# Kernel optimization log

Measured on AMD Instinct MI355X. Metric: run time of the kernel, lower is better.

Reference implementation:

```python
import jax, jax.numpy as jnp
import numpy as np

B, T, S, H = 8, 256, 256, 512


def setup_inputs() -> dict:
    key = jax.random.key(0)
    k1, k2, k3, k4, k5, k6, k7 = jax.random.split(key, 7)
    query = jax.random.normal(k1, (B, T, H), dtype=jnp.float32)
    encoder_outputs = jax.random.normal(k2, (B, S, H), dtype=jnp.float32)
    src_lengths = jax.random.randint(k3, (B,), 1, S + 1)
    src_lengths = src_lengths.at[0].set(S)  # ensure max(lengths) == S (torch code masks to lengths.max())
    scale = 1.0 / np.sqrt(H)
    W_s = jax.random.normal(k4, (H, H), dtype=jnp.float32) * scale      # nn.Linear(H,H) weight
    W_h = jax.random.normal(k5, (H, H), dtype=jnp.float32) * scale
    v = jax.random.normal(k6, (H,), dtype=jnp.float32) * scale          # nn.Linear(H,1) weight
    W_out = jax.random.normal(k7, (H, 2 * H), dtype=jnp.float32) * scale  # nn.Linear(2H,H) weight
    return {"query": query, "encoder_outputs": encoder_outputs, "src_lengths": src_lengths,
            "W_s": W_s, "W_h": W_h, "v": v, "W_out": W_out}


def reference(query, encoder_outputs, src_lengths, W_s, W_h, v, W_out):
    # torch Linear: y = x @ W.T
    Ws_q = jnp.einsum('bth,oh->bto', query, W_s)            # (B,T,H)
    Wh_e = jnp.einsum('bsh,oh->bso', encoder_outputs, W_h)  # (B,S,H)
    # score(i,j) = v^T tanh(Ws_q_j + Wh_e_i), broadcast over (B,T,S,H)
    energies = jnp.einsum('btsh,h->bts',
                          jnp.tanh(Ws_q[:, :, None, :] + Wh_e[:, None, :, :]), v)
    mask = jnp.arange(encoder_outputs.shape[1]) < src_lengths[:, None]  # (B,S)
    energies = jnp.where(mask[:, None, :], energies, -jnp.inf)
    attn_weights = jax.nn.softmax(energies, axis=-1)        # (B,T,S)
    context = jnp.einsum('bts,bsh->bth', attn_weights, encoder_outputs)
    combined = jnp.concatenate([context, query], axis=-1)   # (B,T,2H)
    attn_out = jnp.tanh(jnp.einsum('btk,ok->bto', combined, W_out))
    return attn_out
```

## Files before the change

### kernel.cpp

```cpp
#include <hip/hip_runtime.h>
#include <hip/hip_bf16.h>


typedef __attribute__((ext_vector_type(8))) short bf16x8;
typedef __attribute__((ext_vector_type(4))) float floatx4;

#define C2LOG2E 2.8853900817779268f
#define LOG2E   1.4426950408889634f
#define NEGBIG  -1e30f

__device__ __forceinline__ float fexp2(float x) { return __builtin_amdgcn_exp2f(x); }
__device__ __forceinline__ float frcp(float x)  { return __builtin_amdgcn_rcpf(x); }
__device__ __forceinline__ float ftanh(float x) {
    return 1.0f - 2.0f * frcp(1.0f + fexp2(C2LOG2E * x));
}

__device__ __forceinline__ unsigned int f2bf_bits(float f) {
    unsigned int u = __float_as_uint(f);
    return (u + 0x7fffu + ((u >> 16) & 1u)) >> 16;
}

__global__ __launch_bounds__(256) void cast_all_bf16(
    const float* __restrict__ q,  const float* __restrict__ e,
    const float* __restrict__ Ws, const float* __restrict__ Wh,
    const float* __restrict__ Wo,
    unsigned short* __restrict__ qb,  unsigned short* __restrict__ eb,
    unsigned short* __restrict__ Wsb, unsigned short* __restrict__ Whb,
    unsigned short* __restrict__ Wob)
{
    int blk = blockIdx.x;
    const float* src; unsigned short* dst; int base;
    if      (blk < 1024) { src = q;  dst = qb;  base = blk; }
    else if (blk < 2048) { src = e;  dst = eb;  base = blk - 1024; }
    else if (blk < 2304) { src = Ws; dst = Wsb; base = blk - 2048; }
    else if (blk < 2560) { src = Wh; dst = Whb; base = blk - 2304; }
    else                 { src = Wo; dst = Wob; base = blk - 2560; }
    size_t i = (size_t)base * 1024 + threadIdx.x * 4;
    float4 f = *(const float4*)(src + i);
    ushort4 o;
    o.x = (unsigned short)f2bf_bits(f.x);
    o.y = (unsigned short)f2bf_bits(f.y);
    o.z = (unsigned short)f2bf_bits(f.z);
    o.w = (unsigned short)f2bf_bits(f.w);
    *(ushort4*)(dst + i) = o;
}

__global__ __launch_bounds__(256) void gemm32x64_tanh_dual(
    const unsigned short* __restrict__ Xa, const unsigned short* __restrict__ Wa,
    float* __restrict__ Ca,
    const unsigned short* __restrict__ Xb, const unsigned short* __restrict__ Wb_,
    float* __restrict__ Cb)
{
    __shared__ unsigned short sA[32 * 72];
    __shared__ unsigned short sB[64 * 72];
    const int K = 512;
    int blk = blockIdx.x;
    const unsigned short* X; const unsigned short* W; float* C;
    int mt, nt, N;
    if (blk < 512) { X = Xa; W = Wa; C = Ca; N = 512;  mt = blk >> 3; nt = blk & 7; }
    else { blk -= 512; X = Xb; W = Wb_; C = Cb; N = 2048; mt = blk >> 5; nt = blk & 31; }
    int row0 = mt * 32, col0 = nt * 64;
    int tid = threadIdx.x, lane = tid & 63, w = tid >> 6;
    int srA = tid >> 3, scA = (tid & 7) * 8;
    int srB = tid >> 2, scB = (tid & 3) * 16;
    int mw = (w & 1) * 16, nw = (w >> 1) * 32;
    int r = lane & 15, kq = (lane >> 4) * 8;

    floatx4 acc0 = {0,0,0,0}, acc1 = {0,0,0,0};
    const unsigned short* ga = X + (size_t)(row0 + srA) * K + scA;
    const unsigned short* gb = W + (size_t)(col0 + srB) * K + scB;

    for (int kb = 0; kb < 8; ++kb) {
        uint4 a0 = *(const uint4*)(ga);
        uint4 b0 = *(const uint4*)(gb);
        uint4 b1 = *(const uint4*)(gb + 8);
        ga += 64; gb += 64;
        __syncthreads();
        *(uint4*)&sA[srA * 72 + scA]     = a0;
        *(uint4*)&sB[srB * 72 + scB]     = b0;
        *(uint4*)&sB[srB * 72 + scB + 8] = b1;
        __syncthreads();
#pragma unroll
        for (int ks = 0; ks < 64; ks += 32) {
            bf16x8 af  = *(const bf16x8*)&sA[(mw + r) * 72 + ks + kq];
            bf16x8 bf0 = *(const bf16x8*)&sB[(nw + r) * 72 + ks + kq];
            bf16x8 bf1 = *(const bf16x8*)&sB[(nw + 16 + r) * 72 + ks + kq];
            acc0 = __builtin_amdgcn_mfma_f32_16x16x32_bf16(af, bf0, acc0, 0, 0, 0);
            acc1 = __builtin_amdgcn_mfma_f32_16x16x32_bf16(af, bf1, acc1, 0, 0, 0);
        }
    }
    int rq = (lane >> 4) * 4;
    float* cp = C + (size_t)(row0 + mw + rq) * N + col0 + nw + r;
#pragma unroll
    for (int i = 0; i < 4; ++i) {
        cp[(size_t)i * N]      = ftanh(acc0[i]);
        cp[(size_t)i * N + 16] = ftanh(acc1[i]);
    }
}

#define TQ 4
__global__ __launch_bounds__(512) void energies_v3(
    const float* __restrict__ Aq,
    const float* __restrict__ BhT,
    const float* __restrict__ Vv,
    const int* __restrict__ Len,
    float* __restrict__ E)
{
    __shared__ float sA[TQ][516];
    __shared__ float sV[512];
    __shared__ float sRed[8][TQ][66];

    int tid  = threadIdx.x;
    int lane = tid & 63;
    int w    = tid >> 6;
    int blk  = blockIdx.x;
    int b    = blk >> 8;
    int j    = (blk >> 6) & 3;
    int tq   = blk & 63;
    int len  = Len[b];
    if (j * 64 >= len) return;
    int row0g = b * 256 + tq * TQ;

    {
        int t = tid >> 7, c = (tid & 127) * 4;
        *(float4*)&sA[t][c] = *(const float4*)(Aq + (size_t)(row0g + t) * 512 + c);
        sV[tid] = Vv[tid];
    }
    __syncthreads();

    int h0 = w * 64;
    float acc[TQ] = {0.f, 0.f, 0.f, 0.f};
    const float* bt = BhT + (size_t)h0 * 2048 + b * 256 + j * 64 + lane;

    float B0 = bt[0], B1 = bt[2048], B2 = bt[2 * 2048], B3 = bt[3 * 2048];
#pragma unroll
    for (int hh = 0; hh < 64; hh += 4) {
        float P0, P1, P2, P3;
        if (hh + 4 < 64) {
            const float* nb = bt + (size_t)(hh + 4) * 2048;
            P0 = nb[0]; P1 = nb[2048]; P2 = nb[2 * 2048]; P3 = nb[3 * 2048];
        }
        float4 v4 = *(const float4*)&sV[h0 + hh];
#pragma unroll
        for (int t = 0; t < TQ; ++t) {
            float4 a4 = *(const float4*)&sA[t][h0 + hh];
            float n0 = a4.x + B0, n1 = a4.y + B1;
            float n2 = a4.z + B2, n3 = a4.w + B3;
            float d0 = fmaf(a4.x, B0, 1.0f), d1 = fmaf(a4.y, B1, 1.0f);
            float d2 = fmaf(a4.z, B2, 1.0f), d3 = fmaf(a4.w, B3, 1.0f);
            float x0 = v4.x * n0, x1 = v4.y * n1;
            float x2 = v4.z * n2, x3 = v4.w * n3;
            float num01 = fmaf(x1, d0, x0 * d1);
            float num23 = fmaf(x3, d2, x2 * d3);
            acc[t] = fmaf(num01, frcp(d0 * d1), acc[t]);
            acc[t] = fmaf(num23, frcp(d2 * d3), acc[t]);
        }
        B0 = P0; B1 = P1; B2 = P2; B3 = P3;
    }

#pragma unroll
    for (int t = 0; t < TQ; ++t) sRed[w][t][lane] = acc[t];
    __syncthreads();
    if (tid < 256) {
        int t = tid >> 6, s = tid & 63;
        float sum = 0.f;
#pragma unroll
        for (int ww = 0; ww < 8; ++ww) sum += sRed[ww][t][s];
        E[(size_t)(row0g + t) * 256 + j * 64 + s] = sum;
    }
}

__global__ __launch_bounds__(512) void softmax_ctx_fused(
    const float* __restrict__ E,
    const unsigned short* __restrict__ Eb,
    const int* __restrict__ Len,
    unsigned short* __restrict__ Ctx)
{
    __shared__ unsigned short EncT[64][264];
    __shared__ unsigned short sWb[64][264];
    int tid = threadIdx.x, lane = tid & 63, w = tid >> 6;
    int blk = blockIdx.x;
    int b = blk & 7, hq = (blk >> 3) & 7, tg = blk >> 6;
    int len = Len[b];

    {
        int s = tid >> 1, hg = (tid & 1) * 32;
        const ushort4* src = (const ushort4*)(Eb + (size_t)(b * 256 + s) * 512 + hq * 64 + hg);
#pragma unroll
        for (int k = 0; k < 8; ++k) {
            ushort4 u = src[k];
            EncT[hg + k * 4 + 0][s] = u.x;
            EncT[hg + k * 4 + 1][s] = u.y;
            EncT[hg + k * 4 + 2][s] = u.z;
            EncT[hg + k * 4 + 3][s] = u.w;
        }
    }
    for (int i = 0; i < 8; ++i) {
        int row = w * 8 + i;
        const float* erow = E + (size_t)(b * 256 + tg * 64 + row) * 256;
        float ev[4];
#pragma unroll
        for (int j = 0; j < 4; ++j) {
            int s = lane + 64 * j;
            ev[j] = (s < len) ? erow[s] : NEGBIG;
        }
        float m = fmaxf(fmaxf(ev[0], ev[1]), fmaxf(ev[2], ev[3]));
#pragma unroll
        for (int o = 1; o < 64; o <<= 1) m = fmaxf(m, __shfl_xor(m, o, 64));
        float wv[4], wsum = 0.f;
#pragma unroll
        for (int j = 0; j < 4; ++j) { wv[j] = fexp2((ev[j] - m) * LOG2E); wsum += wv[j]; }
#pragma unroll
        for (int o = 1; o < 64; o <<= 1) wsum += __shfl_xor(wsum, o, 64);
        float inv = frcp(wsum);
#pragma unroll
        for (int j = 0; j < 4; ++j)
            sWb[row][lane + 64 * j] = (unsigned short)f2bf_bits(wv[j] * inv);
    }
    __syncthreads();

    int mt = w & 3, npair = w >> 2;
    int t0 = mt * 16;
    int r  = lane & 15, kq = (lane >> 4) * 8;
    int n0 = npair * 32 + r;
    floatx4 acc0 = {0.f,0.f,0.f,0.f}, acc1 = {0.f,0.f,0.f,0.f};
#pragma unroll
    for (int k = 0; k < 8; ++k) {
        bf16x8 a  = *(const bf16x8*)(&sWb[t0 + r][kq + 32 * k]);
        bf16x8 b0 = *(const bf16x8*)(&EncT[n0][kq + 32 * k]);
        bf16x8 b1 = *(const bf16x8*)(&EncT[n0 + 16][kq + 32 * k]);
        acc0 = __builtin_amdgcn_mfma_f32_16x16x32_bf16(a, b0, acc0, 0, 0, 0);
        acc1 = __builtin_amdgcn_mfma_f32_16x16x32_bf16(a, b1, acc1, 0, 0, 0);
    }
    int row0 = (lane >> 4) * 4;
    unsigned short* op = Ctx + (size_t)(b * 256 + tg * 64 + t0 + row0) * 512 + hq * 64 + npair * 32 + r;
#pragma unroll
    for (int i = 0; i < 4; ++i) {
        op[i * 512]      = (unsigned short)f2bf_bits(acc0[i]);
        op[i * 512 + 16] = (unsigned short)f2bf_bits(acc1[i]);
    }
}

__global__ __launch_bounds__(256) void out_gemm32x64_tanh(
    const unsigned short* __restrict__ Ctx, const unsigned short* __restrict__ Q,
    const unsigned short* __restrict__ Wout, float* __restrict__ Out)
{
    __shared__ unsigned short sA[32 * 72];
    __shared__ unsigned short sB[64 * 72];
    const int N = 512, KW = 1024;
    int blk = blockIdx.x;
    int mt = blk >> 3, nt = blk & 7;
    int row0 = mt * 32, col0 = nt * 64;
    int tid = threadIdx.x, lane = tid & 63, w = tid >> 6;
    int srA = tid >> 3, scA = (tid & 7) * 8;
    int srB = tid >> 2, scB = (tid & 3) * 16;
    int mw = (w & 1) * 16, nw = (w >> 1) * 32;
    int r = lane & 15, kq = (lane >> 4) * 8;

    floatx4 acc0 = {0,0,0,0}, acc1 = {0,0,0,0};
    const unsigned short* gb = Wout + (size_t)(col0 + srB) * KW + scB;

    for (int kb = 0; kb < 16; ++kb) {
        const unsigned short* asrc = (kb < 8 ? Ctx : Q);
        const unsigned short* ga = asrc + (size_t)(row0 + srA) * 512 + (kb & 7) * 64 + scA;
        uint4 a0 = *(const uint4*)(ga);
        uint4 b0 = *(const uint4*)(gb);
        uint4 b1 = *(const uint4*)(gb + 8);
        gb += 64;
        __syncthreads();
        *(uint4*)&sA[srA * 72 + scA]     = a0;
        *(uint4*)&sB[srB * 72 + scB]     = b0;
        *(uint4*)&sB[srB * 72 + scB + 8] = b1;
        __syncthreads();
#pragma unroll
        for (int ks = 0; ks < 64; ks += 32) {
            bf16x8 af  = *(const bf16x8*)&sA[(mw + r) * 72 + ks + kq];
            bf16x8 bf0 = *(const bf16x8*)&sB[(nw + r) * 72 + ks + kq];
            bf16x8 bf1 = *(const bf16x8*)&sB[(nw + 16 + r) * 72 + ks + kq];
            acc0 = __builtin_amdgcn_mfma_f32_16x16x32_bf16(af, bf0, acc0, 0, 0, 0);
            acc1 = __builtin_amdgcn_mfma_f32_16x16x32_bf16(af, bf1, acc1, 0, 0, 0);
        }
    }
    int rq = (lane >> 4) * 4;
    float* op = Out + (size_t)(row0 + mw + rq) * N + col0 + nw + r;
#pragma unroll
    for (int i = 0; i < 4; ++i) {
        op[(size_t)i * N]      = ftanh(acc0[i]);
        op[(size_t)i * N + 16] = ftanh(acc1[i]);
    }
}

extern "C" void kernel_launch(void* const* d_in, const int* in_sizes, int n_in,
                              void* d_out, int out_size, void* d_ws, size_t ws_size,
                              hipStream_t stream)
{
    const float* query = (const float*)d_in[0];
    const float* enc   = (const float*)d_in[1];
    const int*   len   = (const int*)d_in[2];
    const float* Ws    = (const float*)d_in[3];
    const float* Wh    = (const float*)d_in[4];
    const float* v     = (const float*)d_in[5];
    const float* Wout  = (const float*)d_in[6];
    float* out = (float*)d_out;

    float* wsq  = (float*)d_ws;
    float* wheT = wsq + 2048 * 512;
    float* E    = wheT + 512 * 2048;
    unsigned short* qb  = (unsigned short*)(E + 2048 * 256);
    unsigned short* eb  = qb + 2048 * 512;
    unsigned short* Wsb = eb + 2048 * 512;
    unsigned short* Whb = Wsb + 512 * 512;
    unsigned short* Wob = Whb + 512 * 512;
    unsigned short* ctx = Wob + 512 * 1024;

    cast_all_bf16<<<3072, 256, 0, stream>>>(query, enc, Ws, Wh, Wout,
                                            qb, eb, Wsb, Whb, Wob);
    gemm32x64_tanh_dual<<<1024, 256, 0, stream>>>(qb, Wsb, wsq, Whb, eb, wheT);
    energies_v3<<<2048, 512, 0, stream>>>(wsq, wheT, v, len, E);
    softmax_ctx_fused<<<256, 512, 0, stream>>>(E, eb, len, ctx);
    out_gemm32x64_tanh<<<512, 256, 0, stream>>>(ctx, qb, Wob, out);
}
```

Measured before the change: 129.2 us.

## Reformulate energies with exponentials and double query rows per block

The projection GEMM epilogue now stores exp(2x) instead of tanh(x). The energy kernel then uses tanh(a+b) = 1 - 2/(1+e^{2a}e^{2b}), which drops the row-constant sum of v because softmax ignores it. That cuts the per-element arithmetic to one FMA denominator and a cheaper numerator using pre-scaled -2v weights. The energy tile also grows from 4 to 8 query rows per block, halving the grid and reusing each loaded encoder value across more rows. The exponential form risks overflow for large projections, and the larger accumulator array adds register pressure.

```diff
diff --git a/kernel.cpp b/kernel.cpp
--- a/kernel.cpp
+++ b/kernel.cpp
@@ -13,6 +13,9 @@
 __device__ __forceinline__ float frcp(float x)  { return __builtin_amdgcn_rcpf(x); }
 __device__ __forceinline__ float ftanh(float x) {
     return 1.0f - 2.0f * frcp(1.0f + fexp2(C2LOG2E * x));
+}
+__device__ __forceinline__ float fexp2x(float x) {
+    return fexp2(C2LOG2E * x);
 }
 
 __device__ __forceinline__ unsigned int f2bf_bits(float f) {
@@ -45,7 +48,7 @@
     *(ushort4*)(dst + i) = o;
 }
 
-__global__ __launch_bounds__(256) void gemm32x64_tanh_dual(
+__global__ __launch_bounds__(256) void gemm32x64_exp_dual(
     const unsigned short* __restrict__ Xa, const unsigned short* __restrict__ Wa,
     float* __restrict__ Ca,
     const unsigned short* __restrict__ Xb, const unsigned short* __restrict__ Wb_,
@@ -93,44 +96,46 @@
     float* cp = C + (size_t)(row0 + mw + rq) * N + col0 + nw + r;
 #pragma unroll
     for (int i = 0; i < 4; ++i) {
-        cp[(size_t)i * N]      = ftanh(acc0[i]);
-        cp[(size_t)i * N + 16] = ftanh(acc1[i]);
-    }
-}
-
-#define TQ 4
-__global__ __launch_bounds__(512) void energies_v3(
-    const float* __restrict__ Aq,
-    const float* __restrict__ BhT,
+        cp[(size_t)i * N]      = fexp2x(acc0[i]);
+        cp[(size_t)i * N + 16] = fexp2x(acc1[i]);
+    }
+}
+
+#define TQ 8
+__global__ __launch_bounds__(512) void energies_v4(
+    const float* __restrict__ EA,
+    const float* __restrict__ EBT,
     const float* __restrict__ Vv,
     const int* __restrict__ Len,
     float* __restrict__ E)
 {
     __shared__ float sA[TQ][516];
-    __shared__ float sV[512];
+    __shared__ float sWn[512];
     __shared__ float sRed[8][TQ][66];
 
     int tid  = threadIdx.x;
     int lane = tid & 63;
     int w    = tid >> 6;
     int blk  = blockIdx.x;
-    int b    = blk >> 8;
-    int j    = (blk >> 6) & 3;
-    int tq   = blk & 63;
+    int b    = blk >> 7;
+    int j    = (blk >> 5) & 3;
+    int tq   = blk & 31;
     int len  = Len[b];
     if (j * 64 >= len) return;
     int row0g = b * 256 + tq * TQ;
 
     {
-        int t = tid >> 7, c = (tid & 127) * 4;
-        *(float4*)&sA[t][c] = *(const float4*)(Aq + (size_t)(row0g + t) * 512 + c);
-        sV[tid] = Vv[tid];
+        int t = tid >> 6, c = (tid & 63) * 8;
+        const float* src = EA + (size_t)(row0g + t) * 512 + c;
+        *(float4*)&sA[t][c]     = *(const float4*)(src);
+        *(float4*)&sA[t][c + 4] = *(const float4*)(src + 4);
+        sWn[tid] = -2.0f * Vv[tid];
     }
     __syncthreads();
 
     int h0 = w * 64;
-    float acc[TQ] = {0.f, 0.f, 0.f, 0.f};
-    const float* bt = BhT + (size_t)h0 * 2048 + b * 256 + j * 64 + lane;
+    float acc[TQ] = {0.f, 0.f, 0.f, 0.f, 0.f, 0.f, 0.f, 0.f};
+    const float* bt = EBT + (size_t)h0 * 2048 + b * 256 + j * 64 + lane;
 
     float B0 = bt[0], B1 = bt[2048], B2 = bt[2 * 2048], B3 = bt[3 * 2048];
 #pragma unroll
@@ -140,18 +145,14 @@
             const float* nb = bt + (size_t)(hh + 4) * 2048;
             P0 = nb[0]; P1 = nb[2048]; P2 = nb[2 * 2048]; P3 = nb[3 * 2048];
         }
-        float4 v4 = *(const float4*)&sV[h0 + hh];
+        float4 w4 = *(const float4*)&sWn[h0 + hh];
 #pragma unroll
         for (int t = 0; t < TQ; ++t) {
             float4 a4 = *(const float4*)&sA[t][h0 + hh];
-            float n0 = a4.x + B0, n1 = a4.y + B1;
-            float n2 = a4.z + B2, n3 = a4.w + B3;
             float d0 = fmaf(a4.x, B0, 1.0f), d1 = fmaf(a4.y, B1, 1.0f);
             float d2 = fmaf(a4.z, B2, 1.0f), d3 = fmaf(a4.w, B3, 1.0f);
-            float x0 = v4.x * n0, x1 = v4.y * n1;
-            float x2 = v4.z * n2, x3 = v4.w * n3;
-            float num01 = fmaf(x1, d0, x0 * d1);
-            float num23 = fmaf(x3, d2, x2 * d3);
+            float num01 = fmaf(w4.x, d1, w4.y * d0);
+            float num23 = fmaf(w4.z, d3, w4.w * d2);
             acc[t] = fmaf(num01, frcp(d0 * d1), acc[t]);
             acc[t] = fmaf(num23, frcp(d2 * d3), acc[t]);
         }
@@ -161,7 +162,7 @@
 #pragma unroll
     for (int t = 0; t < TQ; ++t) sRed[w][t][lane] = acc[t];
     __syncthreads();
-    if (tid < 256) {
+    {
         int t = tid >> 6, s = tid & 63;
         float sum = 0.f;
 #pragma unroll
@@ -303,9 +304,9 @@
     const float* Wout  = (const float*)d_in[6];
     float* out = (float*)d_out;
 
-    float* wsq  = (float*)d_ws;
-    float* wheT = wsq + 2048 * 512;
-    float* E    = wheT + 512 * 2048;
+    float* EA   = (float*)d_ws;
+    float* EBT  = EA + 2048 * 512;
+    float* E    = EBT + 512 * 2048;
     unsigned short* qb  = (unsigned short*)(E + 2048 * 256);
     unsigned short* eb  = qb + 2048 * 512;
     unsigned short* Wsb = eb + 2048 * 512;
@@ -315,8 +316,8 @@
 
     cast_all_bf16<<<3072, 256, 0, stream>>>(query, enc, Ws, Wh, Wout,
                                             qb, eb, Wsb, Whb, Wob);
-    gemm32x64_tanh_dual<<<1024, 256, 0, stream>>>(qb, Wsb, wsq, Whb, eb, wheT);
-    energies_v3<<<2048, 512, 0, stream>>>(wsq, wheT, v, len, E);
+    gemm32x64_exp_dual<<<1024, 256, 0, stream>>>(qb, Wsb, EA, Whb, eb, EBT);
+    energies_v4<<<1024, 512, 0, stream>>>(EA, EBT, v, len, E);
     softmax_ctx_fused<<<256, 512, 0, stream>>>(E, eb, len, ctx);
     out_gemm32x64_tanh<<<512, 256, 0, stream>>>(ctx, qb, Wob, out);
 }
```

Result: faster. 126.3 us (-2.3%).
